# Kernel tuning notes

Measured on AMD Instinct MI355X. Metric: run time of the kernel, lower is better.

## Reference

```python
import jax, jax.numpy as jnp
import numpy as np

N = 50000      # nodes
E = 800000     # edges (before self loops)
F_IN = 128     # dataset.num_features
HID = 32       # hidden_channels (per GAT head)
HEADS = 4
C = 40         # dataset.num_classes
NEG_SLOPE = 0.2


def setup_inputs() -> dict:
    key = jax.random.key(0)
    ks = jax.random.split(key, 18)
    g = lambda k, shape, fan: jax.random.normal(k, shape, dtype=jnp.float32) / np.sqrt(fan)
    inp = {
        "x": jax.random.normal(ks[0], (N, F_IN), dtype=jnp.float32),
        "edge_index": jax.random.randint(ks[1], (2, E), 0, N, dtype=jnp.int64),
        # GAT layer 1: F_IN -> HEADS*HID
        "gat_W1": g(ks[2], (F_IN, HEADS * HID), F_IN),
        "gat_att_src1": g(ks[3], (HEADS, HID), HID),
        "gat_att_dst1": g(ks[4], (HEADS, HID), HID),
        "gat_b1": jnp.zeros((HEADS * HID,), jnp.float32),
        # GAT layer 2: HEADS*HID -> C, heads=1
        "gat_W2": g(ks[5], (HEADS * HID, C), HEADS * HID),
        "gat_att_src2": g(ks[6], (1, C), C),
        "gat_att_dst2": g(ks[7], (1, C), C),
        "gat_b2": jnp.zeros((C,), jnp.float32),
        # GCN layers
        "gcn_W1": g(ks[8], (F_IN, HID), F_IN),
        "gcn_b1": jnp.zeros((HID,), jnp.float32),
        "gcn_W2": g(ks[9], (HID, C), HID),
        "gcn_b2": jnp.zeros((C,), jnp.float32),
        # final linear: 2C -> C
        "lin_W": g(ks[10], (2 * C, C), 2 * C),
        "lin_b": jnp.zeros((C,), jnp.float32),
        "weight_c": jnp.float32(0.5),
        "weight_t": jnp.float32(0.5),
    }
    return inp


def _add_self_loops(src, dst, n):
    loop = jnp.arange(n, dtype=src.dtype)
    return jnp.concatenate([src, loop]), jnp.concatenate([dst, loop])


def _gat_conv(x, src, dst, n, W, att_src, att_dst, b, heads, out_dim):
    # h: [n, heads, out_dim]
    h = (x @ W).reshape(n, heads, out_dim)
    a_s = jnp.einsum('nhd,hd->nh', h, att_src)   # source-side attention logit
    a_d = jnp.einsum('nhd,hd->nh', h, att_dst)   # target-side attention logit
    e = jax.nn.leaky_relu(a_s[src] + a_d[dst], NEG_SLOPE)  # [E', heads]
    # softmax over incoming edges of each target node (self loops guarantee >=1 edge)
    m = jax.ops.segment_max(e, dst, num_segments=n)
    ex = jnp.exp(e - m[dst])
    s = jax.ops.segment_sum(ex, dst, num_segments=n)
    alpha = ex / s[dst]                          # [E', heads]
    out = jax.ops.segment_sum(h[src] * alpha[..., None], dst, num_segments=n)
    return out.reshape(n, heads * out_dim) + b


def _gcn_conv(x, src, dst, n, W, b):
    h = x @ W
    deg = jax.ops.segment_sum(jnp.ones(src.shape, h.dtype), dst, num_segments=n)
    norm = jax.lax.rsqrt(deg)                    # deg >= 1 (self loops)
    coef = (norm[src] * norm[dst])[:, None]
    return jax.ops.segment_sum(h[src] * coef, dst, num_segments=n) + b


def reference(x, edge_index, gat_W1, gat_att_src1, gat_att_dst1, gat_b1,
              gat_W2, gat_att_src2, gat_att_dst2, gat_b2,
              gcn_W1, gcn_b1, gcn_W2, gcn_b2, lin_W, lin_b,
              weight_c, weight_t):
    n = x.shape[0]
    src, dst = _add_self_loops(edge_index[0], edge_index[1], n)
    # GAT branch (dropout is identity at inference)
    x_gat = _gat_conv(x, src, dst, n, gat_W1, gat_att_src1, gat_att_dst1,
                      gat_b1, HEADS, HID)
    x_gat = jax.nn.elu(x_gat)
    x_gat = _gat_conv(x_gat, src, dst, n, gat_W2, gat_att_src2, gat_att_dst2,
                      gat_b2, 1, C)
    # GCN branch
    x_gcn = jax.nn.relu(_gcn_conv(x, src, dst, n, gcn_W1, gcn_b1))
    x_gcn = _gcn_conv(x_gcn, src, dst, n, gcn_W2, gcn_b2)
    # weighted feature concat + linear head
    cat = jnp.concatenate([x_gcn * weight_c, x_gat * weight_t], axis=1)  # [n, 2C]
    return cat @ lin_W + lin_b
```

## Files before the change

kernel.cpp:

```cpp
#include <hip/hip_runtime.h>
#include <math.h>

#define F_IN   128
#define HIDC   32
#define NHEAD  4
#define CDIM   40
#define NEG_SLOPE 0.2f
#define BCAP   4096
#define OVCAP  16384
#define SCHUNK 4096

typedef __attribute__((ext_vector_type(8))) short bf16x8;
typedef __attribute__((ext_vector_type(4))) float f32x4;

__device__ __forceinline__ float leakyf(float x) { return x > 0.f ? x : NEG_SLOPE * x; }

__device__ __forceinline__ float wred_sum(float v) {
#pragma unroll
    for (int o = 32; o > 0; o >>= 1) v += __shfl_xor(v, o, 64);
    return v;
}
__device__ __forceinline__ float sel4(float4 v, int h) {
    return (h == 0) ? v.x : (h == 1) ? v.y : (h == 2) ? v.z : v.w;
}
__device__ __forceinline__ unsigned pack2_bf16(float a, float b) {
    unsigned ua = __float_as_uint(a);
    unsigned ub = __float_as_uint(b);
    ua = (ua + 0x7FFFu + ((ua >> 16) & 1u)) >> 16;
    ub = (ub + 0x7FFFu + ((ub >> 16) & 1u)) >> 16;
    return ua | (ub << 16);
}
__device__ __forceinline__ float2 unpack2_bf16(unsigned p) {
    return make_float2(__uint_as_float(p << 16), __uint_as_float(p & 0xFFFF0000u));
}
__device__ __forceinline__ float bf2f(unsigned short u) {
    return __uint_as_float(((unsigned)u) << 16);
}

__global__ void wb_prep_kernel(const float* __restrict__ Wg, const float* __restrict__ Wc,
                               uint4* __restrict__ wbf)
{
    int b = blockIdx.x;
    int lane = threadIdx.x;
    int nt = b >> 2, ks = b & 3;
    int c = nt * 16 + (lane & 15);
    int k0 = ks * 32 + (lane >> 4) * 8;
    unsigned u[4];
#pragma unroll
    for (int jj = 0; jj < 4; ++jj) {
        int k = k0 + 2 * jj;
        float a0 = (c < 128) ? Wg[(size_t)k * 128 + c] : Wc[(size_t)k * 32 + (c - 128)];
        float a1 = (c < 128) ? Wg[(size_t)(k + 1) * 128 + c] : Wc[(size_t)(k + 1) * 32 + (c - 128)];
        u[jj] = pack2_bf16(a0, a1);
    }
    wbf[(size_t)b * 64 + lane] = make_uint4(u[0], u[1], u[2], u[3]);
}

__global__ __launch_bounds__(256) void gemm1_mfma_kernel(
    const float* __restrict__ X, const uint4* __restrict__ wbf,
    const float* __restrict__ aw_s, const float* __restrict__ aw_d,
    unsigned* __restrict__ h1b, unsigned* __restrict__ g1b,
    float* __restrict__ as1, float* __restrict__ ad1, int n)
{
    __shared__ float Ct[64][164];
    __shared__ float sw[128], dw[128];
    const int tid = threadIdx.x;
    const int w = tid >> 6, lane = tid & 63;
    const int m = lane & 15, q = lane >> 4;
    const int node0 = blockIdx.x * 64;
    if (tid < 128) { sw[tid] = aw_s[tid]; dw[tid] = aw_d[tid]; }

    f32x4 acc[10];
#pragma unroll
    for (int t = 0; t < 10; ++t) acc[t] = (f32x4){0.f, 0.f, 0.f, 0.f};

    const int row = node0 + w * 16 + m;
    const bool rv = row < n;
#pragma unroll
    for (int ks = 0; ks < 4; ++ks) {
        uint4 pa = make_uint4(0u, 0u, 0u, 0u);
        if (rv) {
            const float* xr = X + (size_t)row * 128 + ks * 32 + q * 8;
            float4 a0 = *(const float4*)xr;
            float4 a1 = *(const float4*)(xr + 4);
            pa = make_uint4(pack2_bf16(a0.x, a0.y), pack2_bf16(a0.z, a0.w),
                            pack2_bf16(a1.x, a1.y), pack2_bf16(a1.z, a1.w));
        }
        bf16x8 af = *(bf16x8*)&pa;
#pragma unroll
        for (int nt = 0; nt < 10; ++nt) {
            uint4 pb = wbf[(size_t)(nt * 4 + ks) * 64 + lane];
            bf16x8 bfv = *(bf16x8*)&pb;
            acc[nt] = __builtin_amdgcn_mfma_f32_16x16x32_bf16(af, bfv, acc[nt], 0, 0, 0);
        }
    }
#pragma unroll
    for (int nt = 0; nt < 10; ++nt)
#pragma unroll
        for (int r = 0; r < 4; ++r)
            Ct[w * 16 + q * 4 + r][nt * 16 + m] = acc[nt][r];
    __syncthreads();

    for (int i = tid; i < 64 * 64; i += 256) {
        int nd = i >> 6, u = i & 63;
        int gn = node0 + nd;
        if (gn < n)
            h1b[(size_t)gn * 64 + u] = pack2_bf16(Ct[nd][2 * u], Ct[nd][2 * u + 1]);
    }
    for (int i = tid; i < 64 * 16; i += 256) {
        int nd = i >> 4, u = i & 15;
        int gn = node0 + nd;
        if (gn < n)
            g1b[(size_t)gn * 16 + u] = pack2_bf16(Ct[nd][128 + 2 * u], Ct[nd][128 + 2 * u + 1]);
    }
    {
        int nd = tid >> 2, h = tid & 3;
        int gn = node0 + nd;
        if (gn < n) {
            float s = 0.f, d = 0.f;
#pragma unroll
            for (int k = 0; k < HIDC; ++k) {
                float v = Ct[nd][h * HIDC + k];
                s = fmaf(v, sw[h * HIDC + k], s);
                d = fmaf(v, dw[h * HIDC + k], d);
            }
            as1[(size_t)gn * 4 + h] = s;
            ad1[(size_t)gn * 4 + h] = d;
        }
    }
}

template<int K, int OUTC, int BN, int BK, int OSTRIDE = OUTC>
__global__ __launch_bounds__((OUTC / 4) * (BN / 4)) void gemm_tile(
    const float* __restrict__ X, const float* __restrict__ W,
    const float* __restrict__ bias, float* __restrict__ Y, int n)
{
    constexpr int CG = OUTC / 4;
    constexpr int NG = BN / 4;
    constexpr int NT = CG * NG;
    __shared__ float Xs[BK][BN + 4];
    __shared__ float Ws[BK][OUTC];
    const int tid = threadIdx.x;
    const int cg = tid % CG, ng = tid / CG;
    const int node0 = blockIdx.x * BN;
    float acc[4][4] = {};

    for (int kb = 0; kb < K; kb += BK) {
        for (int idx = tid; idx < BN * (BK / 4); idx += NT) {
            int nd = idx / (BK / 4);
            int kq = idx % (BK / 4);
            int gnode = node0 + nd;
            float4 v = (gnode < n) ? *(const float4*)&X[(size_t)gnode * K + kb + kq * 4]
                                   : make_float4(0.f, 0.f, 0.f, 0.f);
            Xs[kq * 4 + 0][nd] = v.x;
            Xs[kq * 4 + 1][nd] = v.y;
            Xs[kq * 4 + 2][nd] = v.z;
            Xs[kq * 4 + 3][nd] = v.w;
        }
        for (int idx = tid; idx < BK * CG; idx += NT) {
            int kk = idx / CG;
            int cq = idx % CG;
            *(float4*)&Ws[kk][cq * 4] = *(const float4*)&W[(size_t)(kb + kk) * OUTC + cq * 4];
        }
        __syncthreads();
#pragma unroll
        for (int k = 0; k < BK; ++k) {
            float4 xv = *(const float4*)&Xs[k][ng * 4];
            float4 wv = *(const float4*)&Ws[k][cg * 4];
            float xa[4] = {xv.x, xv.y, xv.z, xv.w};
            float wa[4] = {wv.x, wv.y, wv.z, wv.w};
#pragma unroll
            for (int j = 0; j < 4; ++j)
#pragma unroll
                for (int c = 0; c < 4; ++c)
                    acc[j][c] = fmaf(xa[j], wa[c], acc[j][c]);
        }
        __syncthreads();
    }

    float4 bv = make_float4(0.f, 0.f, 0.f, 0.f);
    if (bias) bv = *(const float4*)&bias[cg * 4];
#pragma unroll
    for (int j = 0; j < 4; ++j) {
        int gnode = node0 + ng * 4 + j;
        if (gnode < n) {
            float4 o = make_float4(acc[j][0] + bv.x, acc[j][1] + bv.y,
                                   acc[j][2] + bv.z, acc[j][3] + bv.w);
            *(float4*)&Y[(size_t)gnode * OSTRIDE + cg * 4] = o;
        }
    }
}

template<int K, int OUTC, int BN, int BK, int OSTRIDE_U, int OFF_U>
__global__ __launch_bounds__((OUTC / 4) * (BN / 4)) void gemm_tile_bb(
    const unsigned* __restrict__ Xb, const float* __restrict__ W,
    unsigned* __restrict__ Yb, int n)
{
    constexpr int CG = OUTC / 4;
    constexpr int NG = BN / 4;
    constexpr int NT = CG * NG;
    __shared__ float Xs[BK][BN + 4];
    __shared__ float Ws[BK][OUTC];
    const int tid = threadIdx.x;
    const int cg = tid % CG, ng = tid / CG;
    const int node0 = blockIdx.x * BN;
    float acc[4][4] = {};

    for (int kb = 0; kb < K; kb += BK) {
        for (int idx = tid; idx < BN * (BK / 8); idx += NT) {
            int nd = idx / (BK / 8);
            int kq = idx % (BK / 8);
            int gnode = node0 + nd;
            uint4 v = (gnode < n) ? *(const uint4*)&Xb[(size_t)gnode * (K / 2) + kb / 2 + kq * 4]
                                  : make_uint4(0u, 0u, 0u, 0u);
            float2 a = unpack2_bf16(v.x), b = unpack2_bf16(v.y);
            float2 c = unpack2_bf16(v.z), d = unpack2_bf16(v.w);
            Xs[kq * 8 + 0][nd] = a.x; Xs[kq * 8 + 1][nd] = a.y;
            Xs[kq * 8 + 2][nd] = b.x; Xs[kq * 8 + 3][nd] = b.y;
            Xs[kq * 8 + 4][nd] = c.x; Xs[kq * 8 + 5][nd] = c.y;
            Xs[kq * 8 + 6][nd] = d.x; Xs[kq * 8 + 7][nd] = d.y;
        }
        for (int idx = tid; idx < BK * CG; idx += NT) {
            int kk = idx / CG;
            int cq = idx % CG;
            *(float4*)&Ws[kk][cq * 4] = *(const float4*)&W[(size_t)(kb + kk) * OUTC + cq * 4];
        }
        __syncthreads();
#pragma unroll
        for (int k = 0; k < BK; ++k) {
            float4 xv = *(const float4*)&Xs[k][ng * 4];
            float4 wv = *(const float4*)&Ws[k][cg * 4];
            float xa[4] = {xv.x, xv.y, xv.z, xv.w};
            float wa[4] = {wv.x, wv.y, wv.z, wv.w};
#pragma unroll
            for (int j = 0; j < 4; ++j)
#pragma unroll
                for (int c = 0; c < 4; ++c)
                    acc[j][c] = fmaf(xa[j], wa[c], acc[j][c]);
        }
        __syncthreads();
    }

#pragma unroll
    for (int j = 0; j < 4; ++j) {
        int gnode = node0 + ng * 4 + j;
        if (gnode < n) {
            uint2 pb = make_uint2(pack2_bf16(acc[j][0], acc[j][1]),
                                  pack2_bf16(acc[j][2], acc[j][3]));
            *(uint2*)&Yb[(size_t)gnode * OSTRIDE_U + OFF_U + cg * 2] = pb;
        }
    }
}

__global__ __launch_bounds__(320) void gemm2_gat_kernel(
    const unsigned* __restrict__ Xb, const float* __restrict__ W,
    const float* __restrict__ aw_s, const float* __restrict__ aw_d,
    unsigned* __restrict__ Yb, float* __restrict__ as2, float* __restrict__ ad2, int n)
{
    constexpr int K = 128, OUTC = 40, BN = 128, BK = 32;
    constexpr int CG = OUTC / 4, NT = 320;
    __shared__ float smem[32 * 132 + 32 * 40];
    float* Xs = smem;
    float* Ws = smem + 32 * 132;
    const int tid = threadIdx.x;
    const int cg = tid % CG, ng = tid / CG;
    const int node0 = blockIdx.x * BN;
    float acc[4][4] = {};

    for (int kb = 0; kb < K; kb += BK) {
        for (int idx = tid; idx < BN * (BK / 8); idx += NT) {
            int nd = idx / (BK / 8);
            int kq = idx % (BK / 8);
            int gnode = node0 + nd;
            uint4 v = (gnode < n) ? *(const uint4*)&Xb[(size_t)gnode * (K / 2) + kb / 2 + kq * 4]
                                  : make_uint4(0u, 0u, 0u, 0u);
            float2 a = unpack2_bf16(v.x), b = unpack2_bf16(v.y);
            float2 c = unpack2_bf16(v.z), d = unpack2_bf16(v.w);
            Xs[(kq * 8 + 0) * 132 + nd] = a.x; Xs[(kq * 8 + 1) * 132 + nd] = a.y;
            Xs[(kq * 8 + 2) * 132 + nd] = b.x; Xs[(kq * 8 + 3) * 132 + nd] = b.y;
            Xs[(kq * 8 + 4) * 132 + nd] = c.x; Xs[(kq * 8 + 5) * 132 + nd] = c.y;
            Xs[(kq * 8 + 6) * 132 + nd] = d.x; Xs[(kq * 8 + 7) * 132 + nd] = d.y;
        }
        for (int idx = tid; idx < BK * CG; idx += NT) {
            int kk = idx / CG;
            int cq = idx % CG;
            *(float4*)&Ws[kk * 40 + cq * 4] = *(const float4*)&W[(size_t)(kb + kk) * OUTC + cq * 4];
        }
        __syncthreads();
#pragma unroll
        for (int k = 0; k < BK; ++k) {
            float4 xv = *(const float4*)&Xs[k * 132 + ng * 4];
            float4 wv = *(const float4*)&Ws[k * 40 + cg * 4];
            float xa[4] = {xv.x, xv.y, xv.z, xv.w};
            float wa[4] = {wv.x, wv.y, wv.z, wv.w};
#pragma unroll
            for (int j = 0; j < 4; ++j)
#pragma unroll
                for (int c = 0; c < 4; ++c)
                    acc[j][c] = fmaf(xa[j], wa[c], acc[j][c]);
        }
        __syncthreads();
    }

    float* Ct  = smem;
    float* sww = smem + 128 * 41;
    float* dww = sww + 40;
#pragma unroll
    for (int j = 0; j < 4; ++j) {
        int gnode = node0 + ng * 4 + j;
        if (gnode < n) {
            uint2 pb = make_uint2(pack2_bf16(acc[j][0], acc[j][1]),
                                  pack2_bf16(acc[j][2], acc[j][3]));
            *(uint2*)&Yb[(size_t)gnode * 40 + cg * 2] = pb;
        }
#pragma unroll
        for (int c = 0; c < 4; ++c)
            Ct[(ng * 4 + j) * 41 + cg * 4 + c] = acc[j][c];
    }
    if (tid < 40) { sww[tid] = aw_s[tid]; dww[tid] = aw_d[tid]; }
    __syncthreads();
    if (tid < 128) {
        int gnode = node0 + tid;
        if (gnode < n) {
            float s = 0.f, d = 0.f;
#pragma unroll
            for (int c = 0; c < 40; ++c) {
                float v = Ct[tid * 41 + c];
                s = fmaf(v, sww[c], s);
                d = fmaf(v, dww[c], d);
            }
            as2[gnode] = s;
            ad2[gnode] = d;
        }
    }
}

__global__ __launch_bounds__(256) void bucket_scatter_kernel(
    const int* __restrict__ src, const int* __restrict__ dst,
    unsigned* __restrict__ bcnt, unsigned* __restrict__ bpair,
    unsigned* __restrict__ ovf_cnt, uint2* __restrict__ ovf, int e, int nbuck)
{
    __shared__ unsigned hist[512];
    __shared__ unsigned base[512];
    const int t = threadIdx.x;
    const int lo = blockIdx.x * SCHUNK;
    const int hi = min(lo + SCHUNK, e);
    for (int i = t; i < nbuck; i += 256) hist[i] = 0;
    __syncthreads();
    for (int i = lo + t; i < hi; i += 256)
        atomicAdd(&hist[((unsigned)dst[i]) >> 7], 1u);
    __syncthreads();
    for (int i = t; i < nbuck; i += 256) {
        unsigned c = hist[i];
        base[i] = c ? atomicAdd(&bcnt[i], c) : 0u;
        hist[i] = 0;
    }
    __syncthreads();
    for (int i = lo + t; i < hi; i += 256) {
        unsigned s = (unsigned)src[i], d = (unsigned)dst[i];
        unsigned b = d >> 7;
        unsigned pos = base[b] + atomicAdd(&hist[b], 1u);
        if (pos < BCAP) bpair[(size_t)b * BCAP + pos] = s | ((d & 127u) << 16);
        else {
            unsigned o = atomicAdd(ovf_cnt, 1u);
            if (o < OVCAP) ovf[o] = make_uint2(s, d);
        }
    }
}

__global__ __launch_bounds__(256) void bucket_count_kernel(
    const unsigned* __restrict__ bcnt, const unsigned* __restrict__ bpair,
    const unsigned* __restrict__ ovf_cnt, const uint2* __restrict__ ovf,
    unsigned* __restrict__ counts, int n)
{
    __shared__ unsigned lc[128];
    const int b = blockIdx.x, base = b << 7;
    if (threadIdx.x < 128) lc[threadIdx.x] = 0;
    __syncthreads();
    unsigned bc = bcnt[b];
    int cnt = (int)(bc < BCAP ? bc : BCAP);
    for (int k = threadIdx.x; k < cnt; k += 256)
        atomicAdd(&lc[bpair[(size_t)b * BCAP + k] >> 16], 1u);
    unsigned oc_u = *ovf_cnt;
    int oc = (int)(oc_u < OVCAP ? oc_u : OVCAP);
    for (int k = threadIdx.x; k < oc; k += 256) {
        uint2 pp = ovf[k];
        if ((int)(pp.y >> 7) == b) atomicAdd(&lc[pp.y & 127u], 1u);
    }
    __syncthreads();
    int i = base + threadIdx.x;
    if (threadIdx.x < 128 && i < n) counts[i] = lc[threadIdx.x];
}

__global__ __launch_bounds__(256) void scan_reduce_kernel(const unsigned* __restrict__ counts,
                                                          unsigned* __restrict__ partials, int n)
{
    __shared__ unsigned sm[256];
    int t = threadIdx.x;
    int i = blockIdx.x * 256 + t;
    unsigned v = (i < n) ? counts[i] : 0u;
    sm[t] = v;
    __syncthreads();
#pragma unroll
    for (int off = 128; off > 0; off >>= 1) {
        if (t < off) sm[t] += sm[t + off];
        __syncthreads();
    }
    if (t == 0) partials[blockIdx.x] = sm[0];
}

__global__ __launch_bounds__(256) void scan_partials_kernel(unsigned* __restrict__ partials,
                                                            unsigned* __restrict__ rs, int nb, int n)
{
    __shared__ unsigned sm[256];
    int t = threadIdx.x;
    unsigned v = (t < nb) ? partials[t] : 0u;
    sm[t] = v;
    __syncthreads();
#pragma unroll
    for (int off = 1; off < 256; off <<= 1) {
        unsigned u = (t >= off) ? sm[t - off] : 0u;
        __syncthreads();
        sm[t] += u;
        __syncthreads();
    }
    if (t < nb) partials[t] = sm[t] - v;
    if (t == 255) rs[n] = sm[255];
}

__global__ __launch_bounds__(256) void scan_write_kernel(const unsigned* __restrict__ counts,
                                                         const unsigned* __restrict__ partials,
                                                         unsigned* __restrict__ rs,
                                                         float* __restrict__ nrm, int n)
{
    __shared__ unsigned sm[256];
    int t = threadIdx.x;
    int i = blockIdx.x * 256 + t;
    unsigned c = (i < n) ? counts[i] : 0u;
    sm[t] = c;
    __syncthreads();
#pragma unroll
    for (int off = 1; off < 256; off <<= 1) {
        unsigned u = (t >= off) ? sm[t - off] : 0u;
        __syncthreads();
        sm[t] += u;
        __syncthreads();
    }
    if (i < n) {
        rs[i] = partials[blockIdx.x] + sm[t] - c;
        nrm[i] = rsqrtf((float)(c + 1u));
    }
}

__global__ __launch_bounds__(256) void bucket_place_kernel(
    const unsigned* __restrict__ bcnt, const unsigned* __restrict__ bpair,
    const unsigned* __restrict__ rs, unsigned* __restrict__ csr_src,
    unsigned* __restrict__ cursor, int n)
{
    __shared__ unsigned lc[128];
    __shared__ unsigned rbase[128];
    const int b = blockIdx.x, base = b << 7;
    if (threadIdx.x < 128) {
        lc[threadIdx.x] = 0;
        int i = base + threadIdx.x;
        rbase[threadIdx.x] = (i < n) ? rs[i] : 0u;
    }
    __syncthreads();
    unsigned bc = bcnt[b];
    int cnt = (int)(bc < BCAP ? bc : BCAP);
    for (int k = threadIdx.x; k < cnt; k += 256) {
        unsigned v = bpair[(size_t)b * BCAP + k];
        unsigned ld = v >> 16;
        unsigned r = atomicAdd(&lc[ld], 1u);
        csr_src[rbase[ld] + r] = v & 0xFFFFu;
    }
    __syncthreads();
    int i = base + threadIdx.x;
    if (threadIdx.x < 128 && i < n) cursor[i] = rbase[threadIdx.x] + lc[threadIdx.x];
}

__global__ void overflow_fill_kernel(const unsigned* __restrict__ ovf_cnt,
                                     const uint2* __restrict__ ovf,
                                     unsigned* __restrict__ cursor,
                                     unsigned* __restrict__ csr_src)
{
    unsigned oc_u = *ovf_cnt;
    int oc = (int)(oc_u < OVCAP ? oc_u : OVCAP);
    for (int k = threadIdx.x; k < oc; k += 256) {
        uint2 pp = ovf[k];
        unsigned pos = atomicAdd(&cursor[pp.y], 1u);
        csr_src[pos] = pp.x;
    }
}

#define CAP1 96
__global__ __launch_bounds__(256) void agg1_fused_kernel(
    const unsigned* __restrict__ h1b, const unsigned short* __restrict__ g1b,
    const float* __restrict__ as1, const float* __restrict__ ad1,
    const float* __restrict__ nrm,
    const unsigned* __restrict__ rs, const unsigned* __restrict__ csr_src,
    const float* __restrict__ gat_b1, const float* __restrict__ gcn_b1,
    unsigned* __restrict__ xgb, unsigned* __restrict__ gaccb, int n)
{
    __shared__ unsigned sidx[4][CAP1];
    __shared__ float    w4[4][CAP1][4];
    __shared__ float    cf[4][CAP1];
    const int wid = threadIdx.x >> 6;
    const int lane = threadIdx.x & 63;
    const int i = blockIdx.x * 4 + wid;
    if (i >= n) return;
    const unsigned beg = rs[i];
    const int deg = (int)(rs[i + 1] - beg);
    const float4* as1v = (const float4*)as1;
    float4 av = as1v[i];
    float4 dv = ((const float4*)ad1)[i];
    const float ni = nrm[i];
    float4 ese = make_float4(__expf(leakyf(av.x + dv.x)), __expf(leakyf(av.y + dv.y)),
                             __expf(leakyf(av.z + dv.z)), __expf(leakyf(av.w + dv.w)));
    float s0 = 0.f, s1 = 0.f, s2 = 0.f, s3 = 0.f;
    for (int k = lane; k < deg; k += 64) {
        unsigned s = csr_src[beg + k];
        float4 a = as1v[s];
        float w0 = __expf(leakyf(a.x + dv.x)), w1 = __expf(leakyf(a.y + dv.y));
        float w2 = __expf(leakyf(a.z + dv.z)), w3 = __expf(leakyf(a.w + dv.w));
        if (k < CAP1) {
            sidx[wid][k] = s;
            w4[wid][k][0] = w0; w4[wid][k][1] = w1;
            w4[wid][k][2] = w2; w4[wid][k][3] = w3;
            cf[wid][k] = nrm[s];
        }
        s0 += w0; s1 += w1; s2 += w2; s3 += w3;
    }
    if (lane == 0) { s0 += ese.x; s1 += ese.y; s2 += ese.z; s3 += ese.w; }
    s0 = wred_sum(s0); s1 = wred_sum(s1); s2 = wred_sum(s2); s3 = wred_sum(s3);
    __threadfence_block();
    const int h = lane >> 4;
    const float advh = sel4(dv, h);
    const float ssh  = sel4(make_float4(s0, s1, s2, s3), h);
    const float wself = sel4(ese, h);
    const bool gact = lane < 32;
    float2 hv = unpack2_bf16(h1b[(size_t)i * 64 + lane]);
    float2 acc = make_float2(hv.x * wself, hv.y * wself);
    float gacc = gact ? bf2f(g1b[(size_t)i * 32 + lane]) * ni * ni : 0.f;
    const int dcB = deg < CAP1 ? deg : CAP1;
    int j = 0;
    for (; j + 4 <= dcB; j += 4) {
        unsigned ss[4]; float ww[4], cc[4];
#pragma unroll
        for (int t = 0; t < 4; ++t) {
            ss[t] = sidx[wid][j + t];
            ww[t] = w4[wid][j + t][h];
            cc[t] = cf[wid][j + t];
        }
        unsigned pv[4];
#pragma unroll
        for (int t = 0; t < 4; ++t) pv[t] = h1b[(size_t)ss[t] * 64 + lane];
        float gv[4];
        if (gact) {
#pragma unroll
            for (int t = 0; t < 4; ++t) gv[t] = bf2f(g1b[(size_t)ss[t] * 32 + lane]);
        }
#pragma unroll
        for (int t = 0; t < 4; ++t) {
            float2 v = unpack2_bf16(pv[t]);
            acc.x = fmaf(v.x, ww[t], acc.x);
            acc.y = fmaf(v.y, ww[t], acc.y);
            if (gact) gacc = fmaf(gv[t], cc[t] * ni, gacc);
        }
    }
    for (; j < dcB; ++j) {
        unsigned s = sidx[wid][j];
        float w = w4[wid][j][h], c = cf[wid][j];
        float2 v = unpack2_bf16(h1b[(size_t)s * 64 + lane]);
        acc.x = fmaf(v.x, w, acc.x);
        acc.y = fmaf(v.y, w, acc.y);
        if (gact) gacc = fmaf(bf2f(g1b[(size_t)s * 32 + lane]), c * ni, gacc);
    }
    for (; j < deg; ++j) {
        unsigned s = csr_src[beg + j];
        float4 a = as1v[s];
        float w = __expf(leakyf(sel4(a, h) + advh));
        float c = nrm[s];
        float2 v = unpack2_bf16(h1b[(size_t)s * 64 + lane]);
        acc.x = fmaf(v.x, w, acc.x);
        acc.y = fmaf(v.y, w, acc.y);
        if (gact) gacc = fmaf(bf2f(g1b[(size_t)s * 32 + lane]), c * ni, gacc);
    }
    float inv = 1.f / ssh;
    int c0 = 2 * lane;
    float o0 = acc.x * inv + gat_b1[c0];
    float o1 = acc.y * inv + gat_b1[c0 + 1];
    o0 = o0 > 0.f ? o0 : __expf(o0) - 1.f;
    o1 = o1 > 0.f ? o1 : __expf(o1) - 1.f;
    xgb[(size_t)i * 64 + lane] = pack2_bf16(o0, o1);
    float go = gact ? fmaxf(gacc + gcn_b1[lane], 0.f) : 0.f;
    float gp = __shfl_xor(go, 1, 64);
    if (gact && (lane & 1) == 0)
        gaccb[(size_t)i * 16 + (lane >> 1)] = pack2_bf16(go, gp);
}

#define CAP2 128
__global__ __launch_bounds__(256) void agg2_fused_kernel(
    const unsigned* __restrict__ hg_b, const float* __restrict__ as2,
    const float* __restrict__ ad2, const float* __restrict__ nrm,
    const unsigned* __restrict__ rs, const unsigned* __restrict__ csr_src,
    const float* __restrict__ gat_b2, const float* __restrict__ gcn_b2,
    const float* __restrict__ wc_p, const float* __restrict__ wt_p,
    float* __restrict__ cat, int n)
{
    __shared__ unsigned sidx[4][CAP2];
    __shared__ float    wgt[4][CAP2];
    __shared__ float    cf [4][CAP2];
    const int wid = threadIdx.x >> 6;
    const int lane = threadIdx.x & 63;
    const int i = blockIdx.x * 4 + wid;
    if (i >= n) return;
    const unsigned beg = rs[i];
    const int deg = (int)(rs[i + 1] - beg);
    const float adv = ad2[i];
    const float eself = __expf(leakyf(as2[i] + adv));
    const float ni = nrm[i];
    float ssum = (lane == 0) ? eself : 0.f;
    for (int k = lane; k < deg; k += 64) {
        unsigned s = csr_src[beg + k];
        float w = __expf(leakyf(as2[s] + adv));
        if (k < CAP2) { sidx[wid][k] = s; wgt[wid][k] = w; cf[wid][k] = nrm[s]; }
        ssum += w;
    }
    ssum = wred_sum(ssum);
    __threadfence_block();
    const bool act   = lane < 40;
    const bool isgat = lane < 20;
    const float selfw = isgat ? eself : ni * ni;
    float2 acc = make_float2(0.f, 0.f);
    if (act) {
        float2 v = unpack2_bf16(hg_b[(size_t)i * 40 + lane]);
        acc.x = v.x * selfw; acc.y = v.y * selfw;
    }
    const int dcB = deg < CAP2 ? deg : CAP2;
    int j = 0;
    for (; j + 4 <= dcB; j += 4) {
        unsigned ss[4]; float ww[4];
#pragma unroll
        for (int t = 0; t < 4; ++t) {
            ss[t] = sidx[wid][j + t];
            ww[t] = isgat ? wgt[wid][j + t] : cf[wid][j + t] * ni;
        }
        if (act) {
#pragma unroll
            for (int t = 0; t < 4; ++t) {
                float2 v = unpack2_bf16(hg_b[(size_t)ss[t] * 40 + lane]);
                acc.x = fmaf(v.x, ww[t], acc.x);
                acc.y = fmaf(v.y, ww[t], acc.y);
            }
        }
    }
    for (; j < dcB; ++j) {
        unsigned s = sidx[wid][j];
        float w = isgat ? wgt[wid][j] : cf[wid][j] * ni;
        if (act) {
            float2 v = unpack2_bf16(hg_b[(size_t)s * 40 + lane]);
            acc.x = fmaf(v.x, w, acc.x); acc.y = fmaf(v.y, w, acc.y);
        }
    }
    for (; j < deg; ++j) {
        unsigned s = csr_src[beg + j];
        float w = isgat ? __expf(leakyf(as2[s] + adv)) : nrm[s] * ni;
        if (act) {
            float2 v = unpack2_bf16(hg_b[(size_t)s * 40 + lane]);
            acc.x = fmaf(v.x, w, acc.x); acc.y = fmaf(v.y, w, acc.y);
        }
    }
    if (act) {
        if (isgat) {
            float inv = 1.f / ssum, wt = *wt_p;
            int c0 = 2 * lane;
            cat[(size_t)i * 80 + 40 + c0]     = (acc.x * inv + gat_b2[c0]) * wt;
            cat[(size_t)i * 80 + 40 + c0 + 1] = (acc.y * inv + gat_b2[c0 + 1]) * wt;
        } else {
            float wc = *wc_p;
            int c0 = 2 * (lane - 20);
            cat[(size_t)i * 80 + c0]     = (acc.x + gcn_b2[c0]) * wc;
            cat[(size_t)i * 80 + c0 + 1] = (acc.y + gcn_b2[c0 + 1]) * wc;
        }
    }
}

extern "C" void kernel_launch(void* const* d_in, const int* in_sizes, int n_in,
                              void* d_out, int out_size, void* d_ws, size_t ws_size,
                              hipStream_t stream)
{
    const float* x        = (const float*)d_in[0];
    const int*   eidx     = (const int*)d_in[1];
    const float* gat_W1   = (const float*)d_in[2];
    const float* att_s1   = (const float*)d_in[3];
    const float* att_d1   = (const float*)d_in[4];
    const float* gat_b1   = (const float*)d_in[5];
    const float* gat_W2   = (const float*)d_in[6];
    const float* att_s2   = (const float*)d_in[7];
    const float* att_d2   = (const float*)d_in[8];
    const float* gat_b2   = (const float*)d_in[9];
    const float* gcn_W1   = (const float*)d_in[10];
    const float* gcn_b1   = (const float*)d_in[11];
    const float* gcn_W2   = (const float*)d_in[12];
    const float* gcn_b2   = (const float*)d_in[13];
    const float* lin_W    = (const float*)d_in[14];
    const float* lin_b    = (const float*)d_in[15];
    const float* wc_p     = (const float*)d_in[16];
    const float* wt_p     = (const float*)d_in[17];

    const int n = in_sizes[0] / F_IN;
    const int e = in_sizes[1] / 2;
    const int* src = eidx;
    const int* dst = eidx + e;
    const int NBUCK = (n + 127) >> 7;

    char* p = (char*)d_ws;
    auto alloc = [&](size_t bytes) -> void* {
        void* r = (void*)p;
        p += (bytes + 255) & ~(size_t)255;
        return r;
    };
    unsigned* counts  = (unsigned*)alloc((size_t)n * 4);
    unsigned* rs      = (unsigned*)alloc((size_t)(n + 1) * 4);
    unsigned* cursor  = (unsigned*)alloc((size_t)n * 4);
    unsigned* partials= (unsigned*)alloc(256 * 4);
    unsigned* bcnt    = (unsigned*)alloc((size_t)(NBUCK + 1) * 4);
    unsigned* csr_src = (unsigned*)alloc((size_t)e * 4);
    uint4*    wbf     = (uint4*)alloc(40 * 64 * 16);
    float* nrm     = (float*)alloc((size_t)n * 4);
    float* as1     = (float*)alloc((size_t)n * 4 * 4);
    float* ad1     = (float*)alloc((size_t)n * 4 * 4);
    float* as2     = (float*)alloc((size_t)n * 4);
    float* ad2     = (float*)alloc((size_t)n * 4);
    float* cat     = (float*)alloc((size_t)n * 80 * 4);
    unsigned* hg_b = (unsigned*)alloc((size_t)n * 40 * 4);
    float* xg      = (float*)alloc((size_t)n * F_IN * 4);
    unsigned* g1b  = (unsigned*)alloc((size_t)n * 16 * 4);
    unsigned* gaccb= (unsigned*)alloc((size_t)n * 16 * 4);
    unsigned* bpair = (unsigned*)cat;
    uint2*    ovf   = (uint2*)(bpair + (size_t)NBUCK * BCAP);
    unsigned* h1b   = (unsigned*)cat;
    unsigned* xgb   = (unsigned*)xg;
    unsigned* ovf_cnt = bcnt + NBUCK;

    const int NB = (n + 255) / 256;
    const int WB = (n + 3) / 4;
    const int SB = (e + SCHUNK - 1) / SCHUNK;

    hipMemsetAsync(bcnt, 0, (size_t)(NBUCK + 1) * 4, stream);
    bucket_scatter_kernel<<<SB, 256, 0, stream>>>(src, dst, bcnt, bpair, ovf_cnt, ovf, e, NBUCK);
    bucket_count_kernel<<<NBUCK, 256, 0, stream>>>(bcnt, bpair, ovf_cnt, ovf, counts, n);
    scan_reduce_kernel<<<NB, 256, 0, stream>>>(counts, partials, n);
    scan_partials_kernel<<<1, 256, 0, stream>>>(partials, rs, NB, n);
    scan_write_kernel<<<NB, 256, 0, stream>>>(counts, partials, rs, nrm, n);
    bucket_place_kernel<<<NBUCK, 256, 0, stream>>>(bcnt, bpair, rs, csr_src, cursor, n);
    overflow_fill_kernel<<<1, 256, 0, stream>>>(ovf_cnt, ovf, cursor, csr_src);

    wb_prep_kernel<<<40, 64, 0, stream>>>(gat_W1, gcn_W1, wbf);
    gemm1_mfma_kernel<<<(n + 63) / 64, 256, 0, stream>>>(x, wbf, att_s1, att_d1,
                                                         h1b, g1b, as1, ad1, n);

    agg1_fused_kernel<<<WB, 256, 0, stream>>>(h1b, (const unsigned short*)g1b,
                                              as1, ad1, nrm, rs, csr_src,
                                              gat_b1, gcn_b1, xgb, gaccb, n);

    gemm_tile_bb<32, 40, 128, 32, 40, 20><<<(n + 127) / 128, 320, 0, stream>>>(gaccb, gcn_W2, hg_b, n);
    gemm2_gat_kernel<<<(n + 127) / 128, 320, 0, stream>>>(xgb, gat_W2, att_s2, att_d2,
                                                          hg_b, as2, ad2, n);

    agg2_fused_kernel<<<WB, 256, 0, stream>>>(hg_b, as2, ad2, nrm, rs, csr_src,
                                              gat_b2, gcn_b2, wc_p, wt_p, cat, n);

    gemm_tile<80, 40, 128, 40><<<(n + 127) / 128, 320, 0, stream>>>(cat, lin_W, lin_b, (float*)d_out, n);
}
```

Measured before the change: 305.2 us.

## Interleave GAT/GCN layer-1 features, fuse layer-2 GEMMs, store concat as bf16

After: 313.4 us. 2.7% more time.

```diff
diff --git a/kernel.cpp b/kernel.cpp
--- a/kernel.cpp
+++ b/kernel.cpp
@@ -59,7 +59,7 @@
 __global__ __launch_bounds__(256) void gemm1_mfma_kernel(
     const float* __restrict__ X, const uint4* __restrict__ wbf,
     const float* __restrict__ aw_s, const float* __restrict__ aw_d,
-    unsigned* __restrict__ h1b, unsigned* __restrict__ g1b,
+    unsigned* __restrict__ h1g,
     float* __restrict__ as1, float* __restrict__ ad1, int n)
 {
     __shared__ float Ct[64][164];
@@ -101,17 +101,11 @@
             Ct[w * 16 + q * 4 + r][nt * 16 + m] = acc[nt][r];
     __syncthreads();
 
-    for (int i = tid; i < 64 * 64; i += 256) {
-        int nd = i >> 6, u = i & 63;
+    for (int i = tid; i < 64 * 80; i += 256) {
+        int nd = i / 80, u = i - nd * 80;
         int gn = node0 + nd;
         if (gn < n)
-            h1b[(size_t)gn * 64 + u] = pack2_bf16(Ct[nd][2 * u], Ct[nd][2 * u + 1]);
-    }
-    for (int i = tid; i < 64 * 16; i += 256) {
-        int nd = i >> 4, u = i & 15;
-        int gn = node0 + nd;
-        if (gn < n)
-            g1b[(size_t)gn * 16 + u] = pack2_bf16(Ct[nd][128 + 2 * u], Ct[nd][128 + 2 * u + 1]);
+            h1g[(size_t)gn * 80 + u] = pack2_bf16(Ct[nd][2 * u], Ct[nd][2 * u + 1]);
     }
     {
         int nd = tid >> 2, h = tid & 3;
@@ -126,211 +120,6 @@
             }
             as1[(size_t)gn * 4 + h] = s;
             ad1[(size_t)gn * 4 + h] = d;
-        }
-    }
-}
-
-template<int K, int OUTC, int BN, int BK, int OSTRIDE = OUTC>
-__global__ __launch_bounds__((OUTC / 4) * (BN / 4)) void gemm_tile(
-    const float* __restrict__ X, const float* __restrict__ W,
-    const float* __restrict__ bias, float* __restrict__ Y, int n)
-{
-    constexpr int CG = OUTC / 4;
-    constexpr int NG = BN / 4;
-    constexpr int NT = CG * NG;
-    __shared__ float Xs[BK][BN + 4];
-    __shared__ float Ws[BK][OUTC];
-    const int tid = threadIdx.x;
-    const int cg = tid % CG, ng = tid / CG;
-    const int node0 = blockIdx.x * BN;
-    float acc[4][4] = {};
-
-    for (int kb = 0; kb < K; kb += BK) {
-        for (int idx = tid; idx < BN * (BK / 4); idx += NT) {
-            int nd = idx / (BK / 4);
-            int kq = idx % (BK / 4);
-            int gnode = node0 + nd;
-            float4 v = (gnode < n) ? *(const float4*)&X[(size_t)gnode * K + kb + kq * 4]
-                                   : make_float4(0.f, 0.f, 0.f, 0.f);
-            Xs[kq * 4 + 0][nd] = v.x;
-            Xs[kq * 4 + 1][nd] = v.y;
-            Xs[kq * 4 + 2][nd] = v.z;
-            Xs[kq * 4 + 3][nd] = v.w;
-        }
-        for (int idx = tid; idx < BK * CG; idx += NT) {
-            int kk = idx / CG;
-            int cq = idx % CG;
-            *(float4*)&Ws[kk][cq * 4] = *(const float4*)&W[(size_t)(kb + kk) * OUTC + cq * 4];
-        }
-        __syncthreads();
-#pragma unroll
-        for (int k = 0; k < BK; ++k) {
-            float4 xv = *(const float4*)&Xs[k][ng * 4];
-            float4 wv = *(const float4*)&Ws[k][cg * 4];
-            float xa[4] = {xv.x, xv.y, xv.z, xv.w};
-            float wa[4] = {wv.x, wv.y, wv.z, wv.w};
-#pragma unroll
-            for (int j = 0; j < 4; ++j)
-#pragma unroll
-                for (int c = 0; c < 4; ++c)
-                    acc[j][c] = fmaf(xa[j], wa[c], acc[j][c]);
-        }
-        __syncthreads();
-    }
-
-    float4 bv = make_float4(0.f, 0.f, 0.f, 0.f);
-    if (bias) bv = *(const float4*)&bias[cg * 4];
-#pragma unroll
-    for (int j = 0; j < 4; ++j) {
-        int gnode = node0 + ng * 4 + j;
-        if (gnode < n) {
-            float4 o = make_float4(acc[j][0] + bv.x, acc[j][1] + bv.y,
-                                   acc[j][2] + bv.z, acc[j][3] + bv.w);
-            *(float4*)&Y[(size_t)gnode * OSTRIDE + cg * 4] = o;
-        }
-    }
-}
-
-template<int K, int OUTC, int BN, int BK, int OSTRIDE_U, int OFF_U>
-__global__ __launch_bounds__((OUTC / 4) * (BN / 4)) void gemm_tile_bb(
-    const unsigned* __restrict__ Xb, const float* __restrict__ W,
-    unsigned* __restrict__ Yb, int n)
-{
-    constexpr int CG = OUTC / 4;
-    constexpr int NG = BN / 4;
-    constexpr int NT = CG * NG;
-    __shared__ float Xs[BK][BN + 4];
-    __shared__ float Ws[BK][OUTC];
-    const int tid = threadIdx.x;
-    const int cg = tid % CG, ng = tid / CG;
-    const int node0 = blockIdx.x * BN;
-    float acc[4][4] = {};
-
-    for (int kb = 0; kb < K; kb += BK) {
-        for (int idx = tid; idx < BN * (BK / 8); idx += NT) {
-            int nd = idx / (BK / 8);
-            int kq = idx % (BK / 8);
-            int gnode = node0 + nd;
-            uint4 v = (gnode < n) ? *(const uint4*)&Xb[(size_t)gnode * (K / 2) + kb / 2 + kq * 4]
-                                  : make_uint4(0u, 0u, 0u, 0u);
-            float2 a = unpack2_bf16(v.x), b = unpack2_bf16(v.y);
-            float2 c = unpack2_bf16(v.z), d = unpack2_bf16(v.w);
-            Xs[kq * 8 + 0][nd] = a.x; Xs[kq * 8 + 1][nd] = a.y;
-            Xs[kq * 8 + 2][nd] = b.x; Xs[kq * 8 + 3][nd] = b.y;
-            Xs[kq * 8 + 4][nd] = c.x; Xs[kq * 8 + 5][nd] = c.y;
-            Xs[kq * 8 + 6][nd] = d.x; Xs[kq * 8 + 7][nd] = d.y;
-        }
-        for (int idx = tid; idx < BK * CG; idx += NT) {
-            int kk = idx / CG;
-            int cq = idx % CG;
-            *(float4*)&Ws[kk][cq * 4] = *(const float4*)&W[(size_t)(kb + kk) * OUTC + cq * 4];
-        }
-        __syncthreads();
-#pragma unroll
-        for (int k = 0; k < BK; ++k) {
-            float4 xv = *(const float4*)&Xs[k][ng * 4];
-            float4 wv = *(const float4*)&Ws[k][cg * 4];
-            float xa[4] = {xv.x, xv.y, xv.z, xv.w};
-            float wa[4] = {wv.x, wv.y, wv.z, wv.w};
-#pragma unroll
-            for (int j = 0; j < 4; ++j)
-#pragma unroll
-                for (int c = 0; c < 4; ++c)
-                    acc[j][c] = fmaf(xa[j], wa[c], acc[j][c]);
-        }
-        __syncthreads();
-    }
-
-#pragma unroll
-    for (int j = 0; j < 4; ++j) {
-        int gnode = node0 + ng * 4 + j;
-        if (gnode < n) {
-            uint2 pb = make_uint2(pack2_bf16(acc[j][0], acc[j][1]),
-                                  pack2_bf16(acc[j][2], acc[j][3]));
-            *(uint2*)&Yb[(size_t)gnode * OSTRIDE_U + OFF_U + cg * 2] = pb;
-        }
-    }
-}
-
-__global__ __launch_bounds__(320) void gemm2_gat_kernel(
-    const unsigned* __restrict__ Xb, const float* __restrict__ W,
-    const float* __restrict__ aw_s, const float* __restrict__ aw_d,
-    unsigned* __restrict__ Yb, float* __restrict__ as2, float* __restrict__ ad2, int n)
-{
-    constexpr int K = 128, OUTC = 40, BN = 128, BK = 32;
-    constexpr int CG = OUTC / 4, NT = 320;
-    __shared__ float smem[32 * 132 + 32 * 40];
-    float* Xs = smem;
-    float* Ws = smem + 32 * 132;
-    const int tid = threadIdx.x;
-    const int cg = tid % CG, ng = tid / CG;
-    const int node0 = blockIdx.x * BN;
-    float acc[4][4] = {};
-
-    for (int kb = 0; kb < K; kb += BK) {
-        for (int idx = tid; idx < BN * (BK / 8); idx += NT) {
-            int nd = idx / (BK / 8);
-            int kq = idx % (BK / 8);
-            int gnode = node0 + nd;
-            uint4 v = (gnode < n) ? *(const uint4*)&Xb[(size_t)gnode * (K / 2) + kb / 2 + kq * 4]
-                                  : make_uint4(0u, 0u, 0u, 0u);
-            float2 a = unpack2_bf16(v.x), b = unpack2_bf16(v.y);
-            float2 c = unpack2_bf16(v.z), d = unpack2_bf16(v.w);
-            Xs[(kq * 8 + 0) * 132 + nd] = a.x; Xs[(kq * 8 + 1) * 132 + nd] = a.y;
-            Xs[(kq * 8 + 2) * 132 + nd] = b.x; Xs[(kq * 8 + 3) * 132 + nd] = b.y;
-            Xs[(kq * 8 + 4) * 132 + nd] = c.x; Xs[(kq * 8 + 5) * 132 + nd] = c.y;
-            Xs[(kq * 8 + 6) * 132 + nd] = d.x; Xs[(kq * 8 + 7) * 132 + nd] = d.y;
-        }
-        for (int idx = tid; idx < BK * CG; idx += NT) {
-            int kk = idx / CG;
-            int cq = idx % CG;
-            *(float4*)&Ws[kk * 40 + cq * 4] = *(const float4*)&W[(size_t)(kb + kk) * OUTC + cq * 4];
-        }
-        __syncthreads();
-#pragma unroll
-        for (int k = 0; k < BK; ++k) {
-            float4 xv = *(const float4*)&Xs[k * 132 + ng * 4];
-            float4 wv = *(const float4*)&Ws[k * 40 + cg * 4];
-            float xa[4] = {xv.x, xv.y, xv.z, xv.w};
-            float wa[4] = {wv.x, wv.y, wv.z, wv.w};
-#pragma unroll
-            for (int j = 0; j < 4; ++j)
-#pragma unroll
-                for (int c = 0; c < 4; ++c)
-                    acc[j][c] = fmaf(xa[j], wa[c], acc[j][c]);
-        }
-        __syncthreads();
-    }
-
-    float* Ct  = smem;
-    float* sww = smem + 128 * 41;
-    float* dww = sww + 40;
-#pragma unroll
-    for (int j = 0; j < 4; ++j) {
-        int gnode = node0 + ng * 4 + j;
-        if (gnode < n) {
-            uint2 pb = make_uint2(pack2_bf16(acc[j][0], acc[j][1]),
-                                  pack2_bf16(acc[j][2], acc[j][3]));
-            *(uint2*)&Yb[(size_t)gnode * 40 + cg * 2] = pb;
-        }
-#pragma unroll
-        for (int c = 0; c < 4; ++c)
-            Ct[(ng * 4 + j) * 41 + cg * 4 + c] = acc[j][c];
-    }
-    if (tid < 40) { sww[tid] = aw_s[tid]; dww[tid] = aw_d[tid]; }
-    __syncthreads();
-    if (tid < 128) {
-        int gnode = node0 + tid;
-        if (gnode < n) {
-            float s = 0.f, d = 0.f;
-#pragma unroll
-            for (int c = 0; c < 40; ++c) {
-                float v = Ct[tid * 41 + c];
-                s = fmaf(v, sww[c], s);
-                d = fmaf(v, dww[c], d);
-            }
-            as2[gnode] = s;
-            ad2[gnode] = d;
         }
     }
 }
@@ -495,16 +284,15 @@
 
 #define CAP1 96
 __global__ __launch_bounds__(256) void agg1_fused_kernel(
-    const unsigned* __restrict__ h1b, const unsigned short* __restrict__ g1b,
+    const unsigned* __restrict__ h1g,
     const float* __restrict__ as1, const float* __restrict__ ad1,
     const float* __restrict__ nrm,
     const unsigned* __restrict__ rs, const unsigned* __restrict__ csr_src,
     const float* __restrict__ gat_b1, const float* __restrict__ gcn_b1,
     unsigned* __restrict__ xgb, unsigned* __restrict__ gaccb, int n)
 {
-    __shared__ unsigned sidx[4][CAP1];
-    __shared__ float    w4[4][CAP1][4];
-    __shared__ float    cf[4][CAP1];
+    __shared__ uint2 scA[4][CAP1];
+    __shared__ float w4[4][CAP1][4];
     const int wid = threadIdx.x >> 6;
     const int lane = threadIdx.x & 63;
     const int i = blockIdx.x * 4 + wid;
@@ -524,10 +312,9 @@
         float w0 = __expf(leakyf(a.x + dv.x)), w1 = __expf(leakyf(a.y + dv.y));
         float w2 = __expf(leakyf(a.z + dv.z)), w3 = __expf(leakyf(a.w + dv.w));
         if (k < CAP1) {
-            sidx[wid][k] = s;
+            scA[wid][k] = make_uint2(s, __float_as_uint(nrm[s]));
             w4[wid][k][0] = w0; w4[wid][k][1] = w1;
             w4[wid][k][2] = w2; w4[wid][k][3] = w3;
-            cf[wid][k] = nrm[s];
         }
         s0 += w0; s1 += w1; s2 += w2; s3 += w3;
     }
@@ -539,52 +326,53 @@
     const float ssh  = sel4(make_float4(s0, s1, s2, s3), h);
     const float wself = sel4(ese, h);
     const bool gact = lane < 32;
-    float2 hv = unpack2_bf16(h1b[(size_t)i * 64 + lane]);
+    const unsigned short* h1s = (const unsigned short*)h1g;
+    float2 hv = unpack2_bf16(h1g[(size_t)i * 80 + lane]);
     float2 acc = make_float2(hv.x * wself, hv.y * wself);
-    float gacc = gact ? bf2f(g1b[(size_t)i * 32 + lane]) * ni * ni : 0.f;
+    float gacc = gact ? bf2f(h1s[(size_t)i * 160 + 128 + lane]) * ni * ni : 0.f;
     const int dcB = deg < CAP1 ? deg : CAP1;
     int j = 0;
     for (; j + 4 <= dcB; j += 4) {
-        unsigned ss[4]; float ww[4], cc[4];
+        uint2 sc[4]; float ww[4];
 #pragma unroll
         for (int t = 0; t < 4; ++t) {
-            ss[t] = sidx[wid][j + t];
+            sc[t] = scA[wid][j + t];
             ww[t] = w4[wid][j + t][h];
-            cc[t] = cf[wid][j + t];
         }
         unsigned pv[4];
 #pragma unroll
-        for (int t = 0; t < 4; ++t) pv[t] = h1b[(size_t)ss[t] * 64 + lane];
+        for (int t = 0; t < 4; ++t) pv[t] = h1g[(size_t)sc[t].x * 80 + lane];
         float gv[4];
         if (gact) {
 #pragma unroll
-            for (int t = 0; t < 4; ++t) gv[t] = bf2f(g1b[(size_t)ss[t] * 32 + lane]);
+            for (int t = 0; t < 4; ++t) gv[t] = bf2f(h1s[(size_t)sc[t].x * 160 + 128 + lane]);
         }
 #pragma unroll
         for (int t = 0; t < 4; ++t) {
             float2 v = unpack2_bf16(pv[t]);
             acc.x = fmaf(v.x, ww[t], acc.x);
             acc.y = fmaf(v.y, ww[t], acc.y);
-            if (gact) gacc = fmaf(gv[t], cc[t] * ni, gacc);
+            if (gact) gacc = fmaf(gv[t], __uint_as_float(sc[t].y) * ni, gacc);
         }
     }
     for (; j < dcB; ++j) {
-        unsigned s = sidx[wid][j];
-        float w = w4[wid][j][h], c = cf[wid][j];
-        float2 v = unpack2_bf16(h1b[(size_t)s * 64 + lane]);
+        uint2 sc = scA[wid][j];
+        float w = w4[wid][j][h];
+        float2 v = unpack2_bf16(h1g[(size_t)sc.x * 80 + lane]);
         acc.x = fmaf(v.x, w, acc.x);
         acc.y = fmaf(v.y, w, acc.y);
-        if (gact) gacc = fmaf(bf2f(g1b[(size_t)s * 32 + lane]), c * ni, gacc);
+        if (gact) gacc = fmaf(bf2f(h1s[(size_t)sc.x * 160 + 128 + lane]),
+                              __uint_as_float(sc.y) * ni, gacc);
     }
     for (; j < deg; ++j) {
         unsigned s = csr_src[beg + j];
         float4 a = as1v[s];
         float w = __expf(leakyf(sel4(a, h) + advh));
         float c = nrm[s];
-        float2 v = unpack2_bf16(h1b[(size_t)s * 64 + lane]);
+        float2 v = unpack2_bf16(h1g[(size_t)s * 80 + lane]);
         acc.x = fmaf(v.x, w, acc.x);
         acc.y = fmaf(v.y, w, acc.y);
-        if (gact) gacc = fmaf(bf2f(g1b[(size_t)s * 32 + lane]), c * ni, gacc);
+        if (gact) gacc = fmaf(bf2f(h1s[(size_t)s * 160 + 128 + lane]), c * ni, gacc);
     }
     float inv = 1.f / ssh;
     int c0 = 2 * lane;
@@ -599,6 +387,130 @@
         gaccb[(size_t)i * 16 + (lane >> 1)] = pack2_bf16(go, gp);
 }
 
+__global__ __launch_bounds__(320) void gemm2_fused_kernel(
+    const unsigned* __restrict__ xgb, const unsigned* __restrict__ gaccb,
+    const float* __restrict__ Wgat, const float* __restrict__ Wgcn,
+    const float* __restrict__ aw_s, const float* __restrict__ aw_d,
+    unsigned* __restrict__ hg_b, float* __restrict__ as2, float* __restrict__ ad2, int n)
+{
+    constexpr int BN = 128, NT = 320, CG = 10;
+    __shared__ float smem[32 * 132 + 32 * 40];
+    float* Xs = smem;
+    float* Ws = smem + 32 * 132;
+    const int tid = threadIdx.x;
+    const int cg = tid % CG, ng = tid / CG;
+    const int node0 = blockIdx.x * BN;
+
+    {
+        float acc[4][4] = {};
+        for (int idx = tid; idx < BN * 4; idx += NT) {
+            int nd = idx >> 2, kq = idx & 3;
+            int gnode = node0 + nd;
+            uint4 v = (gnode < n) ? *(const uint4*)&gaccb[(size_t)gnode * 16 + kq * 4]
+                                  : make_uint4(0u, 0u, 0u, 0u);
+            float2 a = unpack2_bf16(v.x), b = unpack2_bf16(v.y);
+            float2 c = unpack2_bf16(v.z), d = unpack2_bf16(v.w);
+            Xs[(kq * 8 + 0) * 132 + nd] = a.x; Xs[(kq * 8 + 1) * 132 + nd] = a.y;
+            Xs[(kq * 8 + 2) * 132 + nd] = b.x; Xs[(kq * 8 + 3) * 132 + nd] = b.y;
+            Xs[(kq * 8 + 4) * 132 + nd] = c.x; Xs[(kq * 8 + 5) * 132 + nd] = c.y;
+            Xs[(kq * 8 + 6) * 132 + nd] = d.x; Xs[(kq * 8 + 7) * 132 + nd] = d.y;
+        }
+        for (int idx = tid; idx < 32 * CG; idx += NT) {
+            int kk = idx / CG, cq = idx % CG;
+            *(float4*)&Ws[kk * 40 + cq * 4] = *(const float4*)&Wgcn[(size_t)kk * 40 + cq * 4];
+        }
+        __syncthreads();
+#pragma unroll
+        for (int k = 0; k < 32; ++k) {
+            float4 xv = *(const float4*)&Xs[k * 132 + ng * 4];
+            float4 wv = *(const float4*)&Ws[k * 40 + cg * 4];
+            float xa[4] = {xv.x, xv.y, xv.z, xv.w};
+            float wa[4] = {wv.x, wv.y, wv.z, wv.w};
+#pragma unroll
+            for (int j = 0; j < 4; ++j)
+#pragma unroll
+                for (int c = 0; c < 4; ++c)
+                    acc[j][c] = fmaf(xa[j], wa[c], acc[j][c]);
+        }
+        __syncthreads();
+#pragma unroll
+        for (int j = 0; j < 4; ++j) {
+            int gnode = node0 + ng * 4 + j;
+            if (gnode < n) {
+                uint2 pb = make_uint2(pack2_bf16(acc[j][0], acc[j][1]),
+                                      pack2_bf16(acc[j][2], acc[j][3]));
+                *(uint2*)&hg_b[(size_t)gnode * 40 + 20 + cg * 2] = pb;
+            }
+        }
+    }
+
+    float acc[4][4] = {};
+    for (int kb = 0; kb < 128; kb += 32) {
+        for (int idx = tid; idx < BN * 4; idx += NT) {
+            int nd = idx >> 2, kq = idx & 3;
+            int gnode = node0 + nd;
+            uint4 v = (gnode < n) ? *(const uint4*)&xgb[(size_t)gnode * 64 + kb / 2 + kq * 4]
+                                  : make_uint4(0u, 0u, 0u, 0u);
+            float2 a = unpack2_bf16(v.x), b = unpack2_bf16(v.y);
+            float2 c = unpack2_bf16(v.z), d = unpack2_bf16(v.w);
+            Xs[(kq * 8 + 0) * 132 + nd] = a.x; Xs[(kq * 8 + 1) * 132 + nd] = a.y;
+            Xs[(kq * 8 + 2) * 132 + nd] = b.x; Xs[(kq * 8 + 3) * 132 + nd] = b.y;
+            Xs[(kq * 8 + 4) * 132 + nd] = c.x; Xs[(kq * 8 + 5) * 132 + nd] = c.y;
+            Xs[(kq * 8 + 6) * 132 + nd] = d.x; Xs[(kq * 8 + 7) * 132 + nd] = d.y;
+        }
+        for (int idx = tid; idx < 32 * CG; idx += NT) {
+            int kk = idx / CG, cq = idx % CG;
+            *(float4*)&Ws[kk * 40 + cq * 4] = *(const float4*)&Wgat[(size_t)(kb + kk) * 40 + cq * 4];
+        }
+        __syncthreads();
+#pragma unroll
+        for (int k = 0; k < 32; ++k) {
+            float4 xv = *(const float4*)&Xs[k * 132 + ng * 4];
+            float4 wv = *(const float4*)&Ws[k * 40 + cg * 4];
+            float xa[4] = {xv.x, xv.y, xv.z, xv.w};
+            float wa[4] = {wv.x, wv.y, wv.z, wv.w};
+#pragma unroll
+            for (int j = 0; j < 4; ++j)
+#pragma unroll
+                for (int c = 0; c < 4; ++c)
+                    acc[j][c] = fmaf(xa[j], wa[c], acc[j][c]);
+        }
+        __syncthreads();
+    }
+
+    float* Ct  = smem;
+    float* sww = smem + 128 * 41;
+    float* dww = sww + 40;
+#pragma unroll
+    for (int j = 0; j < 4; ++j) {
+        int gnode = node0 + ng * 4 + j;
+        if (gnode < n) {
+            uint2 pb = make_uint2(pack2_bf16(acc[j][0], acc[j][1]),
+                                  pack2_bf16(acc[j][2], acc[j][3]));
+            *(uint2*)&hg_b[(size_t)gnode * 40 + cg * 2] = pb;
+        }
+#pragma unroll
+        for (int c = 0; c < 4; ++c)
+            Ct[(ng * 4 + j) * 41 + cg * 4 + c] = acc[j][c];
+    }
+    if (tid < 40) { sww[tid] = aw_s[tid]; dww[tid] = aw_d[tid]; }
+    __syncthreads();
+    if (tid < 128) {
+        int gnode = node0 + tid;
+        if (gnode < n) {
+            float s = 0.f, d = 0.f;
+#pragma unroll
+            for (int c = 0; c < 40; ++c) {
+                float v = Ct[tid * 41 + c];
+                s = fmaf(v, sww[c], s);
+                d = fmaf(v, dww[c], d);
+            }
+            as2[gnode] = s;
+            ad2[gnode] = d;
+        }
+    }
+}
+
 #define CAP2 128
 __global__ __launch_bounds__(256) void agg2_fused_kernel(
     const unsigned* __restrict__ hg_b, const float* __restrict__ as2,
@@ -606,7 +518,7 @@
     const unsigned* __restrict__ rs, const unsigned* __restrict__ csr_src,
     const float* __restrict__ gat_b2, const float* __restrict__ gcn_b2,
     const float* __restrict__ wc_p, const float* __restrict__ wt_p,
-    float* __restrict__ cat, int n)
+    unsigned* __restrict__ catb, int n)
 {
     __shared__ unsigned sidx[4][CAP2];
     __shared__ float    wgt[4][CAP2];
@@ -675,13 +587,72 @@
         if (isgat) {
             float inv = 1.f / ssum, wt = *wt_p;
             int c0 = 2 * lane;
-            cat[(size_t)i * 80 + 40 + c0]     = (acc.x * inv + gat_b2[c0]) * wt;
-            cat[(size_t)i * 80 + 40 + c0 + 1] = (acc.y * inv + gat_b2[c0 + 1]) * wt;
+            catb[(size_t)i * 40 + 20 + lane] =
+                pack2_bf16((acc.x * inv + gat_b2[c0]) * wt,
+                           (acc.y * inv + gat_b2[c0 + 1]) * wt);
         } else {
             float wc = *wc_p;
             int c0 = 2 * (lane - 20);
-            cat[(size_t)i * 80 + c0]     = (acc.x + gcn_b2[c0]) * wc;
-            cat[(size_t)i * 80 + c0 + 1] = (acc.y + gcn_b2[c0 + 1]) * wc;
+            catb[(size_t)i * 40 + (lane - 20)] =
+                pack2_bf16((acc.x + gcn_b2[c0]) * wc,
+                           (acc.y + gcn_b2[c0 + 1]) * wc);
+        }
+    }
+}
+
+__global__ __launch_bounds__(320) void gemm_head_kernel(
+    const unsigned* __restrict__ catb, const float* __restrict__ W,
+    const float* __restrict__ bias, float* __restrict__ out, int n)
+{
+    constexpr int BN = 128, NT = 320, CG = 10, BK = 40;
+    __shared__ float Xs[BK][BN + 4];
+    __shared__ float Ws[BK][40];
+    const int tid = threadIdx.x;
+    const int cg = tid % CG, ng = tid / CG;
+    const int node0 = blockIdx.x * BN;
+    float acc[4][4] = {};
+
+    for (int kb = 0; kb < 80; kb += BK) {
+        for (int idx = tid; idx < BN * 5; idx += NT) {
+            int nd = idx / 5, kq = idx - nd * 5;
+            int gnode = node0 + nd;
+            uint4 v = (gnode < n) ? *(const uint4*)&catb[(size_t)gnode * 40 + kb / 2 + kq * 4]
+                                  : make_uint4(0u, 0u, 0u, 0u);
+            float2 a = unpack2_bf16(v.x), b = unpack2_bf16(v.y);
+            float2 c = unpack2_bf16(v.z), d = unpack2_bf16(v.w);
+            Xs[kq * 8 + 0][nd] = a.x; Xs[kq * 8 + 1][nd] = a.y;
+            Xs[kq * 8 + 2][nd] = b.x; Xs[kq * 8 + 3][nd] = b.y;
+            Xs[kq * 8 + 4][nd] = c.x; Xs[kq * 8 + 5][nd] = c.y;
+            Xs[kq * 8 + 6][nd] = d.x; Xs[kq * 8 + 7][nd] = d.y;
+        }
+        for (int idx = tid; idx < BK * CG; idx += NT) {
+            int kk = idx / CG, cq = idx % CG;
+            *(float4*)&Ws[kk][cq * 4] = *(const float4*)&W[(size_t)(kb + kk) * 40 + cq * 4];
+        }
+        __syncthreads();
+#pragma unroll
+        for (int k = 0; k < BK; ++k) {
+            float4 xv = *(const float4*)&Xs[k][ng * 4];
+            float4 wv = *(const float4*)&Ws[k][cg * 4];
+            float xa[4] = {xv.x, xv.y, xv.z, xv.w};
+            float wa[4] = {wv.x, wv.y, wv.z, wv.w};
+#pragma unroll
+            for (int j = 0; j < 4; ++j)
+#pragma unroll
+                for (int c = 0; c < 4; ++c)
+                    acc[j][c] = fmaf(xa[j], wa[c], acc[j][c]);
+        }
+        __syncthreads();
+    }
+
+    float4 bv = *(const float4*)&bias[cg * 4];
+#pragma unroll
+    for (int j = 0; j < 4; ++j) {
+        int gnode = node0 + ng * 4 + j;
+        if (gnode < n) {
+            float4 o = make_float4(acc[j][0] + bv.x, acc[j][1] + bv.y,
+                                   acc[j][2] + bv.z, acc[j][3] + bv.w);
+            *(float4*)&out[(size_t)gnode * 40 + cg * 4] = o;
         }
     }
 }
@@ -733,15 +704,14 @@
     float* ad1     = (float*)alloc((size_t)n * 4 * 4);
     float* as2     = (float*)alloc((size_t)n * 4);
     float* ad2     = (float*)alloc((size_t)n * 4);
-    float* cat     = (float*)alloc((size_t)n * 80 * 4);
+    unsigned* regA = (unsigned*)alloc((size_t)n * 80 * 4);
     unsigned* hg_b = (unsigned*)alloc((size_t)n * 40 * 4);
-    float* xg      = (float*)alloc((size_t)n * F_IN * 4);
-    unsigned* g1b  = (unsigned*)alloc((size_t)n * 16 * 4);
+    unsigned* xgb  = (unsigned*)alloc((size_t)n * 64 * 4);
     unsigned* gaccb= (unsigned*)alloc((size_t)n * 16 * 4);
-    unsigned* bpair = (unsigned*)cat;
+    unsigned* bpair = regA;
     uint2*    ovf   = (uint2*)(bpair + (size_t)NBUCK * BCAP);
-    unsigned* h1b   = (unsigned*)cat;
-    unsigned* xgb   = (unsigned*)xg;
+    unsigned* h1g   = regA;
+    unsigned* catb  = regA;
     unsigned* ovf_cnt = bcnt + NBUCK;
 
     const int NB = (n + 255) / 256;
@@ -759,18 +729,16 @@
 
     wb_prep_kernel<<<40, 64, 0, stream>>>(gat_W1, gcn_W1, wbf);
     gemm1_mfma_kernel<<<(n + 63) / 64, 256, 0, stream>>>(x, wbf, att_s1, att_d1,
-                                                         h1b, g1b, as1, ad1, n);
-
-    agg1_fused_kernel<<<WB, 256, 0, stream>>>(h1b, (const unsigned short*)g1b,
-                                              as1, ad1, nrm, rs, csr_src,
+                                                         h1g, as1, ad1, n);
+
+    agg1_fused_kernel<<<WB, 256, 0, stream>>>(h1g, as1, ad1, nrm, rs, csr_src,
                                               gat_b1, gcn_b1, xgb, gaccb, n);
 
-    gemm_tile_bb<32, 40, 128, 32, 40, 20><<<(n + 127) / 128, 320, 0, stream>>>(gaccb, gcn_W2, hg_b, n);
-    gemm2_gat_kernel<<<(n + 127) / 128, 320, 0, stream>>>(xgb, gat_W2, att_s2, att_d2,
-                                                          hg_b, as2, ad2, n);
+    gemm2_fused_kernel<<<(n + 127) / 128, 320, 0, stream>>>(xgb, gaccb, gat_W2, gcn_W2,
+                                                            att_s2, att_d2, hg_b, as2, ad2, n);
 
     agg2_fused_kernel<<<WB, 256, 0, stream>>>(hg_b, as2, ad2, nrm, rs, csr_src,
-                                              gat_b2, gcn_b2, wc_p, wt_p, cat, n);
-
-    gemm_tile<80, 40, 128, 40><<<(n + 127) / 128, 320, 0, stream>>>(cat, lin_W, lin_b, (float*)d_out, n);
-}
+                                              gat_b2, gcn_b2, wc_p, wt_p, catb, n);
+
+    gemm_head_kernel<<<(n + 127) / 128, 320, 0, stream>>>(catb, lin_W, lin_b, (float*)d_out, n);
+}
```
